# Optimization experiments

Hardware: AMD Instinct MI355X
Metric: run time of the kernel (lower is better)

The kernel has to match this reference:

```python
import jax, jax.numpy as jnp
import numpy as np

D_MODEL, D_FF, N_EXPERTS, TOP_K = 768, 3072, 8, 2
B, S = 2, 1024
LN_EPS = 1e-5


def setup_inputs() -> dict:
    key = jax.random.key(0)
    k1, k2, k3, k4 = jax.random.split(key, 4)
    return {
        "hidden_states": jax.random.normal(k1, (B, S, D_MODEL), dtype=jnp.float32),
        "ln_gamma": jnp.ones((D_MODEL,), dtype=jnp.float32),
        "ln_beta": jnp.zeros((D_MODEL,), dtype=jnp.float32),
        "router_w": jax.random.normal(k2, (D_MODEL, N_EXPERTS), dtype=jnp.float32) * 0.02,
        "w1": jax.random.normal(k3, (N_EXPERTS, D_MODEL, D_FF), dtype=jnp.float32) * 0.02,
        "w2": jax.random.normal(k4, (N_EXPERTS, D_FF, D_MODEL), dtype=jnp.float32) * 0.02,
    }


def _layernorm(x, gamma, beta):
    mu = jnp.mean(x, axis=-1, keepdims=True)
    var = jnp.mean(jnp.square(x - mu), axis=-1, keepdims=True)
    return (x - mu) * jax.lax.rsqrt(var + LN_EPS) * gamma + beta


def reference(hidden_states, ln_gamma, ln_beta, router_w, w1, w2):
    Bz, Sz, D = hidden_states.shape
    residual = hidden_states
    x = _layernorm(hidden_states, ln_gamma, ln_beta)
    tokens = x.reshape(-1, D)                       # [T, D]
    T = tokens.shape[0]

    # Router: softmax over experts, top-k selection, gate normalization
    logits = tokens @ router_w                      # [T, E]
    probs = jax.nn.softmax(logits, axis=-1)
    topw, topi = jax.lax.top_k(probs, TOP_K)        # [T, K]
    topw = topw / jnp.sum(topw, axis=-1, keepdims=True)  # normalize_gates=True

    # Dense gate matrix [T, E] (zero for unselected experts)
    gates = jnp.zeros((T, N_EXPERTS), dtype=tokens.dtype)
    gates = gates.at[jnp.arange(T)[:, None], topi].set(topw)

    # Per-expert FFN (silu, no bias), weighted combine
    h = jnp.einsum('td,edf->etf', tokens, w1)       # [E, T, F]
    h = jax.nn.silu(h)
    y = jnp.einsum('etf,efd->etd', h, w2)           # [E, T, D]
    out = jnp.einsum('te,etd->td', gates, y)        # [T, D]

    return residual + out.reshape(Bz, Sz, D)
```

## Files before the change

### kernel.cpp

```cpp
#include <hip/hip_runtime.h>
#include <hip/hip_bf16.h>
#include <math.h>

#define T_TOK 2048
#define DM 768
#define DF 3072
#define NE 8
#define NTILES_MAX 40

typedef __attribute__((ext_vector_type(4))) float f32x4;
typedef __attribute__((ext_vector_type(8))) short bf16x8;

static __device__ __forceinline__ ushort f2bf(float f) {
    union { float f; unsigned u; } x; x.f = f;
    unsigned r = x.u + 0x7fff + ((x.u >> 16) & 1);
    return (ushort)(r >> 16);
}
static __device__ __forceinline__ float bf2f(ushort u) {
    union { unsigned u; float f; } x; x.u = ((unsigned)u) << 16; return x.f;
}
static __device__ __forceinline__ unsigned pk2(float lo, float hi) {
    unsigned r;
    asm("v_cvt_pk_bf16_f32 %0, %1, %2" : "=v"(r) : "v"(lo), "v"(hi));
    return r;
}

__global__ __launch_bounds__(256) void ln_router_kernel(
    const float* __restrict__ hs, const float* __restrict__ gamma,
    const float* __restrict__ beta, const float* __restrict__ rw,
    ushort* __restrict__ xbf, float* __restrict__ topw, int* __restrict__ topi,
    int* __restrict__ counts)
{
    int t = blockIdx.x;
    int tid = threadIdx.x;
    const float* row = hs + (size_t)t * DM;
    float v[3];
    v[0] = row[tid]; v[1] = row[tid + 256]; v[2] = row[tid + 512];
    float s  = v[0] + v[1] + v[2];
    float sq = v[0]*v[0] + v[1]*v[1] + v[2]*v[2];
    #pragma unroll
    for (int off = 32; off > 0; off >>= 1) {
        s  += __shfl_down(s, off);
        sq += __shfl_down(sq, off);
    }
    __shared__ float wsum[4], wsq[4];
    __shared__ float pl[4][8];
    int lane = tid & 63, wv = tid >> 6;
    if (lane == 0) { wsum[wv] = s; wsq[wv] = sq; }
    __syncthreads();
    float tot  = wsum[0] + wsum[1] + wsum[2] + wsum[3];
    float totq = wsq[0] + wsq[1] + wsq[2] + wsq[3];
    float mu = tot * (1.0f / 768.0f);
    float var = totq * (1.0f / 768.0f) - mu * mu;
    float rstd = rsqrtf(var + 1e-5f);

    float p[8];
    #pragma unroll
    for (int e = 0; e < 8; e++) p[e] = 0.f;
    #pragma unroll
    for (int i = 0; i < 3; i++) {
        int d = tid + i * 256;
        float yv = (v[i] - mu) * rstd * gamma[d] + beta[d];
        xbf[(size_t)t * DM + d] = f2bf(yv);
        const float* r8 = rw + (size_t)d * 8;
        #pragma unroll
        for (int e = 0; e < 8; e++) p[e] += yv * r8[e];
    }
    #pragma unroll
    for (int off = 32; off > 0; off >>= 1) {
        #pragma unroll
        for (int e = 0; e < 8; e++) p[e] += __shfl_down(p[e], off);
    }
    if (lane == 0) {
        #pragma unroll
        for (int e = 0; e < 8; e++) pl[wv][e] = p[e];
    }
    __syncthreads();
    if (tid == 0) {
        float lg[8];
        #pragma unroll
        for (int e = 0; e < 8; e++) lg[e] = pl[0][e] + pl[1][e] + pl[2][e] + pl[3][e];
        int i0 = 0; float l0 = lg[0];
        #pragma unroll
        for (int e = 1; e < 8; e++) if (lg[e] > l0) { l0 = lg[e]; i0 = e; }
        int i1 = -1; float l1 = -3.4e38f;
        #pragma unroll
        for (int e = 0; e < 8; e++) if (e != i0 && lg[e] > l1) { l1 = lg[e]; i1 = e; }
        float w0 = 1.0f / (1.0f + __expf(l1 - l0));
        topi[2 * t] = i0;  topi[2 * t + 1] = i1;
        topw[2 * t] = w0;  topw[2 * t + 1] = 1.0f - w0;
        atomicAdd(&counts[i0], 1);
        atomicAdd(&counts[i1], 1);
    }
}

__global__ void scan_kernel(int* __restrict__ ctl, int4* __restrict__ tiles)
{
    if (threadIdx.x == 0 && blockIdx.x == 0) {
        int acc = 0, nt = 0;
        for (int e = 0; e < 8; e++) {
            int cnt = ctl[e];
            for (int m0 = 0; m0 < cnt; m0 += 128) {
                tiles[nt] = make_int4(e, acc + m0, min(128, cnt - m0), 0);
                nt++;
            }
            acc += cnt;
        }
        ctl[24] = nt;
    }
}

__global__ __launch_bounds__(256) void bucket_kernel(
    const int* __restrict__ topi, int* __restrict__ ctl,
    int* __restrict__ bucket_tok, int* __restrict__ tok_slot)
{
    int t = blockIdx.x * 256 + threadIdx.x;
    if (t >= T_TOK) return;
    int offs[8]; int acc = 0;
    #pragma unroll
    for (int e = 0; e < 8; e++) { offs[e] = acc; acc += ctl[e]; }
    #pragma unroll
    for (int k = 0; k < 2; k++) {
        int e = topi[2 * t + k];
        int pos = atomicAdd(&ctl[16 + e], 1);
        int idx = offs[e] + pos;
        bucket_tok[idx] = t;
        tok_slot[2 * t + k] = idx;
    }
}

template<bool SILU, bool GATHER, int NT, int SPLITS>
__global__ __launch_bounds__(256) void moe_gemm(
    const ushort* __restrict__ A, const float* __restrict__ W,
    ushort* __restrict__ C, const int* __restrict__ ctl,
    const int* __restrict__ bucket_tok, const int4* __restrict__ tiles,
    int K, int N)
{
    int bid = blockIdx.x;
    int c  = bid % (NT * SPLITS);
    int tl = bid / (NT * SPLITS);
    if (tl >= ctl[24]) return;
    int nt = c % NT;
    int sk = c / NT;
    int4 t4 = tiles[tl];
    int e = t4.x, grow0 = t4.y, rows = t4.z;
    const int Ks = K / SPLITS;
    const int kbase = sk * Ks;

    __shared__ ushort Al[2][128 * 32];
    __shared__ unsigned Bl[2][16 * 128];

    int tid = threadIdx.x, lane = tid & 63, wv = tid >> 6;
    int kchA = ((lane & 3) ^ ((lane >> 3) & 3)) * 8;

    const ushort* aptr[2];
    #pragma unroll
    for (int i = 0; i < 2; i++) {
        int r = i * 64 + wv * 16 + (lane >> 2);
        int rr = r < rows ? r : rows - 1;
        if (GATHER) aptr[i] = A + (size_t)bucket_tok[grow0 + rr] * K;
        else        aptr[i] = A + (size_t)(grow0 + rr) * K;
    }

    const float* Wb = W + (size_t)e * ((size_t)K * N);
    int n0 = nt * 128;
    int rp_[2], cc_[2];
    #pragma unroll
    for (int ii = 0; ii < 2; ii++) {
        int item = wv * 128 + ii * 64 + lane;
        rp_[ii] = item >> 5;
        cc_[ii] = item & 31;
    }

    f32x4 acc[4][4];
    #pragma unroll
    for (int m = 0; m < 4; m++)
        #pragma unroll
        for (int n = 0; n < 4; n++)
            acc[m][n] = (f32x4){0.f, 0.f, 0.f, 0.f};

    int wr = wv >> 1, wc = wv & 1;
    int l15 = lane & 15, kq = lane >> 4;
    int ldstA = (wv * 16) * 32 + lane * 8;
    int xk = (kq & 1) << 4;

    float4 brg[2][2];

    auto stageA = [&](int buf, int k0) {
        #pragma unroll
        for (int i = 0; i < 2; i++) {
            __builtin_amdgcn_global_load_lds(
                (const __attribute__((address_space(1))) void*)(aptr[i] + k0 + kchA),
                (__attribute__((address_space(3))) void*)(&Al[buf][i * 64 * 32 + ldstA]),
                16, 0, 0);
        }
    };
    auto bload = [&](int k0) {
        #pragma unroll
        for (int ii = 0; ii < 2; ii++) {
            const float* s = Wb + (size_t)(k0 + 2 * rp_[ii]) * N + n0 + 4 * cc_[ii];
            brg[ii][0] = *(const float4*)s;
            brg[ii][1] = *(const float4*)(s + N);
        }
    };
    auto bwrite = [&](int buf) {
        #pragma unroll
        for (int ii = 0; ii < 2; ii++) {
            uint4 r;
            r.x = pk2(brg[ii][0].x, brg[ii][1].x);
            r.y = pk2(brg[ii][0].y, brg[ii][1].y);
            r.z = pk2(brg[ii][0].z, brg[ii][1].z);
            r.w = pk2(brg[ii][0].w, brg[ii][1].w);
            *(uint4*)&Bl[buf][rp_[ii] * 128 + ((4 * cc_[ii]) ^ ((rp_[ii] & 7) << 2))] = r;
        }
    };
    auto compute = [&](int cur) {
        bf16x8 af[4], bfr[4];
        #pragma unroll
        for (int m = 0; m < 4; m++) {
            int row = wr * 64 + m * 16 + l15;
            af[m] = *(const bf16x8*)&Al[cur][row * 32 + ((kq ^ ((row >> 1) & 3)) << 3)];
        }
        const unsigned* Blc = &Bl[cur][0];
        #pragma unroll
        for (int n = 0; n < 4; n++) {
            int ncol = wc * 64 + n * 16 + l15;
            union { uint4 u; bf16x8 h; } cvu;
            cvu.u.x = Blc[(kq * 4 + 0) * 128 + (ncol ^ (xk | 0))];
            cvu.u.y = Blc[(kq * 4 + 1) * 128 + (ncol ^ (xk | 4))];
            cvu.u.z = Blc[(kq * 4 + 2) * 128 + (ncol ^ (xk | 8))];
            cvu.u.w = Blc[(kq * 4 + 3) * 128 + (ncol ^ (xk | 12))];
            bfr[n] = cvu.h;
        }
        __builtin_amdgcn_s_setprio(1);
        #pragma unroll
        for (int m = 0; m < 4; m++)
            #pragma unroll
            for (int n = 0; n < 4; n++)
                acc[m][n] = __builtin_amdgcn_mfma_f32_16x16x32_bf16(af[m], bfr[n], acc[m][n], 0, 0, 0);
        __builtin_amdgcn_s_setprio(0);
    };

    const int nk = Ks >> 5;
    stageA(0, kbase);
    bload(kbase);
    asm volatile("s_waitcnt vmcnt(0)" ::: "memory");
    bwrite(0);
    asm volatile("s_waitcnt lgkmcnt(0)" ::: "memory");
    __builtin_amdgcn_s_barrier();

    for (int ks = 0; ks < nk; ks++) {
        int cur = ks & 1;
        bool more = (ks + 1 < nk);
        if (more) {
            stageA(cur ^ 1, kbase + (ks + 1) * 32);
            bload(kbase + (ks + 1) * 32);
        }
        compute(cur);
        if (more) {
            asm volatile("s_waitcnt vmcnt(0)" ::: "memory");
            bwrite(cur ^ 1);
        }
        asm volatile("s_waitcnt vmcnt(0) lgkmcnt(0)" ::: "memory");
        __builtin_amdgcn_s_barrier();
    }

    #pragma unroll
    for (int m = 0; m < 4; m++) {
        #pragma unroll
        for (int n = 0; n < 4; n++) {
            #pragma unroll
            for (int jj = 0; jj < 4; jj++) {
                int r = wr * 64 + m * 16 + kq * 4 + jj;
                if (r < rows) {
                    float v = acc[m][n][jj];
                    if (SILU) v = v / (1.0f + __expf(-v));
                    int col = nt * 128 + wc * 64 + n * 16 + l15;
                    C[((size_t)sk * (T_TOK * 2) + grow0 + r) * N + col] = f2bf(v);
                }
            }
        }
    }
}

template<int SPLITS>
__global__ __launch_bounds__(256) void combine_kernel(
    const float* __restrict__ hs, const ushort* __restrict__ Yp,
    const float* __restrict__ topw, const int* __restrict__ tok_slot,
    float* __restrict__ out)
{
    int t = blockIdx.x, tid = threadIdx.x;
    int s0 = tok_slot[2 * t], s1 = tok_slot[2 * t + 1];
    float w0 = topw[2 * t], w1 = topw[2 * t + 1];
    const float* h = hs + (size_t)t * DM;
    float* o = out + (size_t)t * DM;
    #pragma unroll
    for (int i = 0; i < 3; i++) {
        int d = tid + i * 256;
        float y0 = 0.f, y1 = 0.f;
        #pragma unroll
        for (int s = 0; s < SPLITS; s++) {
            y0 += bf2f(Yp[((size_t)s * (T_TOK * 2) + s0) * DM + d]);
            y1 += bf2f(Yp[((size_t)s * (T_TOK * 2) + s1) * DM + d]);
        }
        o[d] = h[d] + w0 * y0 + w1 * y1;
    }
}

extern "C" void kernel_launch(void* const* d_in, const int* in_sizes, int n_in,
                              void* d_out, int out_size, void* d_ws, size_t ws_size,
                              hipStream_t stream)
{
    const float* hs    = (const float*)d_in[0];
    const float* gamma = (const float*)d_in[1];
    const float* beta  = (const float*)d_in[2];
    const float* rw    = (const float*)d_in[3];
    const float* w1    = (const float*)d_in[4];
    const float* w2    = (const float*)d_in[5];
    float* out = (float*)d_out;
    char* ws = (char*)d_ws;

    size_t o = 0;
    auto alc = [&](size_t b) { size_t r = o; o += (b + 255) & ~255ULL; return r; };
    int*      ctl        = (int*)(ws + alc(256));
    int4*     tiles      = (int4*)(ws + alc(NTILES_MAX * 16));
    float*    topw       = (float*)(ws + alc((size_t)T_TOK * 2 * 4));
    int*      topi       = (int*)(ws + alc((size_t)T_TOK * 2 * 4));
    int*      tok_slot   = (int*)(ws + alc((size_t)T_TOK * 2 * 4));
    int*      bucket_tok = (int*)(ws + alc((size_t)T_TOK * 2 * 4));
    ushort*   xbf        = (ushort*)(ws + alc((size_t)T_TOK * DM * 2));
    ushort*   Hg         = (ushort*)(ws + alc((size_t)T_TOK * 2 * DF * 2));
    size_t yp_off        = alc((size_t)4 * T_TOK * 2 * DM * 2);
    ushort*   Yp         = (ushort*)(ws + yp_off);
    bool can_split       = (o <= ws_size);

    hipMemsetAsync(ctl, 0, 256, stream);
    ln_router_kernel<<<T_TOK, 256, 0, stream>>>(hs, gamma, beta, rw, xbf, topw, topi, ctl);
    scan_kernel<<<1, 64, 0, stream>>>(ctl, tiles);
    bucket_kernel<<<8, 256, 0, stream>>>(topi, ctl, bucket_tok, tok_slot);

    moe_gemm<true, true, 24, 1><<<NTILES_MAX * 24, 256, 0, stream>>>(
        xbf, w1, Hg, ctl, bucket_tok, tiles, DM, DF);

    if (can_split) {
        moe_gemm<false, false, 6, 4><<<NTILES_MAX * 6 * 4, 256, 0, stream>>>(
            Hg, w2, Yp, ctl, bucket_tok, tiles, DF, DM);
        combine_kernel<4><<<T_TOK, 256, 0, stream>>>(hs, Yp, topw, tok_slot, out);
    } else {
        moe_gemm<false, false, 6, 1><<<NTILES_MAX * 6, 256, 0, stream>>>(
            Hg, w2, Yp, ctl, bucket_tok, tiles, DF, DM);
        combine_kernel<1><<<T_TOK, 256, 0, stream>>>(hs, Yp, topw, tok_slot, out);
    }
}
```

Measured before the change: 214.3 us.

## Double MoE GEMM row tile to 256 tokens with 512-thread blocks

Expert row tiles grow from 128 to 256 tokens, and the MoE GEMM blocks grow from 4 to 8 waves, so each block computes a 256x128 output tile. The A-staging and B-staging thread mappings are rewritten so the extra waves share one fp32 weight tile load and bf16 conversion. The aim is to halve how often each expert's fp32 weights are read from memory and converted. In exchange there are fewer blocks to fill the GPU, more padded rows for experts with small token counts, and more LDS per block.

Result: slower. 238.6 us (+11.3%).

```diff
diff --git a/kernel.cpp b/kernel.cpp
--- a/kernel.cpp
+++ b/kernel.cpp
@@ -6,7 +6,7 @@
 #define DM 768
 #define DF 3072
 #define NE 8
-#define NTILES_MAX 40
+#define NTILES_MAX 24
 
 typedef __attribute__((ext_vector_type(4))) float f32x4;
 typedef __attribute__((ext_vector_type(8))) short bf16x8;
@@ -100,8 +100,8 @@
         int acc = 0, nt = 0;
         for (int e = 0; e < 8; e++) {
             int cnt = ctl[e];
-            for (int m0 = 0; m0 < cnt; m0 += 128) {
-                tiles[nt] = make_int4(e, acc + m0, min(128, cnt - m0), 0);
+            for (int m0 = 0; m0 < cnt; m0 += 256) {
+                tiles[nt] = make_int4(e, acc + m0, min(256, cnt - m0), 0);
                 nt++;
             }
             acc += cnt;
@@ -130,7 +130,7 @@
 }
 
 template<bool SILU, bool GATHER, int NT, int SPLITS>
-__global__ __launch_bounds__(256) void moe_gemm(
+__global__ __launch_bounds__(512) void moe_gemm(
     const ushort* __restrict__ A, const float* __restrict__ W,
     ushort* __restrict__ C, const int* __restrict__ ctl,
     const int* __restrict__ bucket_tok, const int4* __restrict__ tiles,
@@ -147,7 +147,7 @@
     const int Ks = K / SPLITS;
     const int kbase = sk * Ks;
 
-    __shared__ ushort Al[2][128 * 32];
+    __shared__ ushort Al[2][256 * 32];
     __shared__ unsigned Bl[2][16 * 128];
 
     int tid = threadIdx.x, lane = tid & 63, wv = tid >> 6;
@@ -156,7 +156,7 @@
     const ushort* aptr[2];
     #pragma unroll
     for (int i = 0; i < 2; i++) {
-        int r = i * 64 + wv * 16 + (lane >> 2);
+        int r = wv * 32 + i * 16 + (lane >> 2);
         int rr = r < rows ? r : rows - 1;
         if (GATHER) aptr[i] = A + (size_t)bucket_tok[grow0 + rr] * K;
         else        aptr[i] = A + (size_t)(grow0 + rr) * K;
@@ -164,13 +164,8 @@
 
     const float* Wb = W + (size_t)e * ((size_t)K * N);
     int n0 = nt * 128;
-    int rp_[2], cc_[2];
-    #pragma unroll
-    for (int ii = 0; ii < 2; ii++) {
-        int item = wv * 128 + ii * 64 + lane;
-        rp_[ii] = item >> 5;
-        cc_[ii] = item & 31;
-    }
+    int rp = tid >> 5;
+    int cc = tid & 31;
 
     f32x4 acc[4][4];
     #pragma unroll
@@ -181,38 +176,31 @@
 
     int wr = wv >> 1, wc = wv & 1;
     int l15 = lane & 15, kq = lane >> 4;
-    int ldstA = (wv * 16) * 32 + lane * 8;
     int xk = (kq & 1) << 4;
 
-    float4 brg[2][2];
+    float4 brg[2];
 
     auto stageA = [&](int buf, int k0) {
         #pragma unroll
         for (int i = 0; i < 2; i++) {
             __builtin_amdgcn_global_load_lds(
                 (const __attribute__((address_space(1))) void*)(aptr[i] + k0 + kchA),
-                (__attribute__((address_space(3))) void*)(&Al[buf][i * 64 * 32 + ldstA]),
+                (__attribute__((address_space(3))) void*)(&Al[buf][(wv * 32 + i * 16) * 32 + lane * 8]),
                 16, 0, 0);
         }
     };
     auto bload = [&](int k0) {
-        #pragma unroll
-        for (int ii = 0; ii < 2; ii++) {
-            const float* s = Wb + (size_t)(k0 + 2 * rp_[ii]) * N + n0 + 4 * cc_[ii];
-            brg[ii][0] = *(const float4*)s;
-            brg[ii][1] = *(const float4*)(s + N);
-        }
+        const float* s = Wb + (size_t)(k0 + 2 * rp) * N + n0 + 4 * cc;
+        brg[0] = *(const float4*)s;
+        brg[1] = *(const float4*)(s + N);
     };
     auto bwrite = [&](int buf) {
-        #pragma unroll
-        for (int ii = 0; ii < 2; ii++) {
-            uint4 r;
-            r.x = pk2(brg[ii][0].x, brg[ii][1].x);
-            r.y = pk2(brg[ii][0].y, brg[ii][1].y);
-            r.z = pk2(brg[ii][0].z, brg[ii][1].z);
-            r.w = pk2(brg[ii][0].w, brg[ii][1].w);
-            *(uint4*)&Bl[buf][rp_[ii] * 128 + ((4 * cc_[ii]) ^ ((rp_[ii] & 7) << 2))] = r;
-        }
+        uint4 r;
+        r.x = pk2(brg[0].x, brg[1].x);
+        r.y = pk2(brg[0].y, brg[1].y);
+        r.z = pk2(brg[0].z, brg[1].z);
+        r.w = pk2(brg[0].w, brg[1].w);
+        *(uint4*)&Bl[buf][rp * 128 + ((4 * cc) ^ ((rp & 7) << 2))] = r;
     };
     auto compute = [&](int cur) {
         bf16x8 af[4], bfr[4];
@@ -339,15 +327,15 @@
     scan_kernel<<<1, 64, 0, stream>>>(ctl, tiles);
     bucket_kernel<<<8, 256, 0, stream>>>(topi, ctl, bucket_tok, tok_slot);
 
-    moe_gemm<true, true, 24, 1><<<NTILES_MAX * 24, 256, 0, stream>>>(
+    moe_gemm<true, true, 24, 1><<<NTILES_MAX * 24, 512, 0, stream>>>(
         xbf, w1, Hg, ctl, bucket_tok, tiles, DM, DF);
 
     if (can_split) {
-        moe_gemm<false, false, 6, 4><<<NTILES_MAX * 6 * 4, 256, 0, stream>>>(
+        moe_gemm<false, false, 6, 4><<<NTILES_MAX * 6 * 4, 512, 0, stream>>>(
             Hg, w2, Yp, ctl, bucket_tok, tiles, DF, DM);
         combine_kernel<4><<<T_TOK, 256, 0, stream>>>(hs, Yp, topw, tok_slot, out);
     } else {
-        moe_gemm<false, false, 6, 1><<<NTILES_MAX * 6, 256, 0, stream>>>(
+        moe_gemm<false, false, 6, 1><<<NTILES_MAX * 6, 512, 0, stream>>>(
             Hg, w2, Yp, ctl, bucket_tok, tiles, DF, DM);
         combine_kernel<1><<<T_TOK, 256, 0, stream>>>(hs, Yp, topw, tok_slot, out);
     }
```
